# Kernel optimization log

Measured on AMD Instinct MI355X. Metric: run time of the kernel, lower is better.

Reference implementation:

```python
import jax, jax.numpy as jnp
import numpy as np

NUM_EMBEDDINGS = 2048
EMBEDDING_DIM = 64
COMMITMENT_COST = 0.25


def setup_inputs() -> dict:
    key = jax.random.key(0)
    k1, k2 = jax.random.split(key)
    inputs = jax.random.normal(k1, (64, 32, 32, EMBEDDING_DIM), dtype=jnp.float32)
    # lecun_uniform-style scale on fan_in = embedding_dim
    limit = np.sqrt(3.0 / EMBEDDING_DIM).astype(np.float32)
    codebook = jax.random.uniform(k2, (EMBEDDING_DIM, NUM_EMBEDDINGS), dtype=jnp.float32,
                                  minval=-limit, maxval=limit)
    return {"inputs": inputs, "codebook": codebook}


def reference(inputs, codebook):
    lax = jax.lax
    flat = jnp.reshape(inputs, (-1, EMBEDDING_DIM))          # [N, D]
    # squared Euclidean distances to each code: [N, K]
    distances = (jnp.sum(jnp.square(flat), 1, keepdims=True)
                 - 2.0 * jnp.matmul(flat, codebook)
                 + jnp.sum(jnp.square(codebook), 0, keepdims=True))
    encoding_indices = jnp.argmin(distances, 1)              # [N]
    flat_q = jnp.take(codebook, encoding_indices, axis=1).swapaxes(1, 0)  # [N, D]
    quantized = jnp.reshape(flat_q, inputs.shape)

    codebook_loss = jnp.mean(jnp.square(quantized - lax.stop_gradient(inputs)))
    commitment_loss = COMMITMENT_COST * jnp.mean(
        jnp.square(lax.stop_gradient(quantized) - inputs))

    encodings = jax.nn.one_hot(encoding_indices, NUM_EMBEDDINGS, dtype=jnp.float32)
    avg_probs = jnp.mean(encodings, 0)
    perplexity = jnp.exp(-jnp.sum(avg_probs * jnp.log(avg_probs + 1e-10)))

    ste = inputs + lax.stop_gradient(quantized - inputs)
    return (ste, perplexity, codebook_loss, commitment_loss)
```

## Files before the change

### kernel.cpp

```cpp
#include <hip/hip_runtime.h>
#include <math.h>

#define KCODES 2048
#define DIM 64
#define NROWS 65536
#define NELEM (NROWS * DIM)

#define WS_HIST 0
#define WS_C2   8192
#define WS_C2S  16384
#define WS_SSE  24576
#define WS_P    32768

#define EPS_PK 33

typedef float  floatx4 __attribute__((ext_vector_type(4)));
typedef short  short8  __attribute__((ext_vector_type(8)));

__device__ __forceinline__ unsigned short f2bf(float f) {
  union { float f; unsigned u; } a; a.f = f;
  unsigned r = (a.u + 0x7FFFu + ((a.u >> 16) & 1u)) >> 16;
  return (unsigned short)r;
}
__device__ __forceinline__ float bf2f(unsigned short h) {
  union { unsigned u; float f; } a; a.u = ((unsigned)h) << 16;
  return a.f;
}

__global__ void vq_colnorm(const float* __restrict__ cb, float* __restrict__ c2,
                           float* __restrict__ c2s) {
  int k = blockIdx.x * 256 + threadIdx.x;
  float s = 0.f;
#pragma unroll
  for (int d = 0; d < DIM; ++d) {
    float v = cb[d * KCODES + k];
    s = fmaf(v, v, s);
  }
  c2[k] = s;
  c2s[k] = (s + 64.0f) * 16384.0f;
}

__global__ void vq_prep(const float* __restrict__ cb, char* __restrict__ P) {
  int tid = blockIdx.x * 256 + threadIdx.x;
  int code = tid & (KCODES - 1);
  int g = tid >> 11;
  short8 hh, ll;
#pragma unroll
  for (int e = 0; e < 8; ++e) {
    float v = -2.0f * cb[(size_t)(g * 8 + e) * KCODES + code];
    unsigned short hb = f2bf(v);
    float lo = v - bf2f(hb);
    hh[e] = (short)hb;
    ll[e] = (short)f2bf(lo);
  }
  int tile = code >> 5;
  int sn = code & 31;
  int pb = g ^ (sn & 7);
  size_t base = (size_t)tile * 8192 + sn * 128 + pb * 16;
  *(short8*)(P + base) = hh;
  *(short8*)(P + base + 4096) = ll;
}

__device__ __forceinline__ void stage_tile(const char* P, char* lds,
                                           int tile, int w, int lane) {
  const char* gp = P + (size_t)tile * 8192 + w * 1024 + lane * 16;
  char* lp = lds + w * 1024 + lane * 16;
  __builtin_amdgcn_global_load_lds(
      (const __attribute__((address_space(1))) unsigned*)gp,
      (__attribute__((address_space(3))) unsigned*)lp, 16, 0, 0);
  __builtin_amdgcn_global_load_lds(
      (const __attribute__((address_space(1))) unsigned*)(gp + 4096),
      (__attribute__((address_space(3))) unsigned*)(lp + 4096), 16, 0, 0);
}

__global__ __launch_bounds__(256, 2) void vq_main(
    const float* __restrict__ inp, const float* __restrict__ cb,
    const float* __restrict__ c2, const float* __restrict__ c2s,
    const char* __restrict__ P, int* __restrict__ hist,
    float* __restrict__ sse, float* __restrict__ out)
{
  __shared__ __align__(16) char Bstage[2][8192];
  __shared__ float s_c2s[KCODES];
  __shared__ int   s_k[128];
  __shared__ int   s_nflag;
  __shared__ int   s_frows[128];
  __shared__ float s_rd[256];
  __shared__ int   s_rk[256];
  __shared__ float s_red[4];

  const int t    = threadIdx.x;
  const int lane = t & 63;
  const int wave = __builtin_amdgcn_readfirstlane(t >> 6);
  const int c    = lane & 15;
  const int q    = lane >> 4;
  const int c7   = c & 7;
  const int rowbase = blockIdx.x * 128 + wave * 32;

  if (t == 0) s_nflag = 0;

#pragma unroll
  for (int i = 0; i < KCODES / 256; ++i) s_c2s[i * 256 + t] = c2s[i * 256 + t];

  short8 Ah[2][2], Al[2][2];
#pragma unroll
  for (int r = 0; r < 2; ++r) {
#pragma unroll
    for (int s = 0; s < 2; ++s) {
      const float* px = inp + (size_t)(rowbase + r * 16 + c) * 64 + s * 32 + q * 8;
      float4 u0 = *(const float4*)px;
      float4 u1 = *(const float4*)(px + 4);
      float u[8] = {u0.x, u0.y, u0.z, u0.w, u1.x, u1.y, u1.z, u1.w};
      short8 hh, ll;
#pragma unroll
      for (int e = 0; e < 8; ++e) {
        float xs = u[e] * 16384.0f;
        unsigned short hb = f2bf(xs);
        float lo = xs - bf2f(hb);
        hh[e] = (short)hb;
        ll[e] = (short)f2bf(lo);
      }
      Ah[r][s] = hh; Al[r][s] = ll;
    }
  }

  unsigned d1[8], d2[8];
#pragma unroll
  for (int i = 0; i < 8; ++i) { d1[i] = 0xFFFFFFFFu; d2[i] = 0xFFFFFFFFu; }

  stage_tile(P, Bstage[0], 0, wave, lane);
  __syncthreads();

  const floatx4 zero = {0.f, 0.f, 0.f, 0.f};

#pragma unroll 2
  for (int j = 0; j < 64; ++j) {
    const int buf = j & 1;
    if (j + 1 < 64) stage_tile(P, Bstage[1 - buf], j + 1, wave, lane);

    float c2v0 = s_c2s[j * 32 + c];
    float c2v1 = s_c2s[j * 32 + 16 + c];

#pragma unroll
    for (int nt = 0; nt < 2; ++nt) {
      const int rowi = nt * 16 + c;
      const char* bp = &Bstage[buf][rowi * 128];
      short8 bh0 = *(const short8*)(bp + ((0 + q) ^ c7) * 16);
      short8 bh1 = *(const short8*)(bp + ((4 + q) ^ c7) * 16);
      short8 bl0 = *(const short8*)(bp + 4096 + ((0 + q) ^ c7) * 16);
      short8 bl1 = *(const short8*)(bp + 4096 + ((4 + q) ^ c7) * 16);
      const float c2v = nt ? c2v1 : c2v0;
      const unsigned kcn = j * 32 + nt * 16 + c;
#pragma unroll
      for (int r = 0; r < 2; ++r) {
        floatx4 acc = __builtin_amdgcn_mfma_f32_16x16x32_bf16(Al[r][1], bh1, zero, 0, 0, 0);
        acc = __builtin_amdgcn_mfma_f32_16x16x32_bf16(Ah[r][1], bl1, acc, 0, 0, 0);
        acc = __builtin_amdgcn_mfma_f32_16x16x32_bf16(Al[r][0], bh0, acc, 0, 0, 0);
        acc = __builtin_amdgcn_mfma_f32_16x16x32_bf16(Ah[r][0], bl0, acc, 0, 0, 0);
        acc = __builtin_amdgcn_mfma_f32_16x16x32_bf16(Ah[r][1], bh1, acc, 0, 0, 0);
        acc = __builtin_amdgcn_mfma_f32_16x16x32_bf16(Ah[r][0], bh0, acc, 0, 0, 0);
#pragma unroll
        for (int reg = 0; reg < 4; ++reg) {
          float dds = acc[reg] + c2v;
          unsigned u = (((unsigned)dds) << 11) + kcn;
          const int i = r * 4 + reg;
          d2[i] = min(d2[i], max(d1[i], u));
          d1[i] = min(d1[i], u);
        }
      }
    }
    __syncthreads();
  }

#pragma unroll
  for (int i = 0; i < 8; ++i) {
    unsigned D1 = d1[i], D2 = d2[i];
#pragma unroll
    for (int off = 1; off < 16; off <<= 1) {
      unsigned o1 = (unsigned)__shfl_xor((int)D1, off, 64);
      unsigned o2 = (unsigned)__shfl_xor((int)D2, off, 64);
      D2 = min(min(D2, o2), max(D1, o1));
      D1 = min(D1, o1);
    }
    if (c == 0) {
      int lrow = wave * 32 + (i >> 2) * 16 + q * 4 + (i & 3);
      s_k[lrow] = (int)(D1 & 2047u);
      if ((int)((D2 >> 11) - (D1 >> 11)) < EPS_PK) {
        int idx = atomicAdd(&s_nflag, 1);
        s_frows[idx] = lrow;
      }
    }
  }
  __syncthreads();

  const int nf = s_nflag;
  for (int f = 0; f < nf; ++f) {
    const int lrow = s_frows[f];
    const float* xr = inp + (size_t)(blockIdx.x * 128 + lrow) * 64;
    float xs[64];
    float x2 = 0.f;
#pragma unroll
    for (int i = 0; i < 16; ++i) {
      float4 v = *(const float4*)(xr + i * 4);
      xs[4 * i + 0] = v.x; xs[4 * i + 1] = v.y; xs[4 * i + 2] = v.z; xs[4 * i + 3] = v.w;
      x2 = fmaf(v.x, v.x, x2); x2 = fmaf(v.y, v.y, x2);
      x2 = fmaf(v.z, v.z, x2); x2 = fmaf(v.w, v.w, x2);
    }
    float dot[8];
#pragma unroll
    for (int cc = 0; cc < 8; ++cc) dot[cc] = 0.f;
    const float* cp = cb + t * 8;
#pragma unroll 4
    for (int d = 0; d < 64; ++d) {
      float xd = xs[d];
#pragma unroll
      for (int cc = 0; cc < 8; ++cc)
        dot[cc] = fmaf(xd, cp[(size_t)d * KCODES + cc], dot[cc]);
    }
    float bd = INFINITY; int bk = 0;
#pragma unroll
    for (int cc = 0; cc < 8; ++cc) {
      float dd = (x2 - 2.0f * dot[cc]) + c2[t * 8 + cc];
      if (dd < bd) { bd = dd; bk = t * 8 + cc; }
    }
    s_rd[t] = bd; s_rk[t] = bk;
    __syncthreads();
    for (int s = 128; s >= 1; s >>= 1) {
      if (t < s) {
        if (s_rd[t + s] < s_rd[t]) { s_rd[t] = s_rd[t + s]; s_rk[t] = s_rk[t + s]; }
      }
      __syncthreads();
    }
    if (t == 0) s_k[lrow] = s_rk[0];
    __syncthreads();
  }

  if (t < 128) atomicAdd(&hist[s_k[t]], 1);

  const int fr = t >> 1;
  const int fd = (t & 1) * 32;
  const int grow = blockIdx.x * 128 + fr;
  const int myk = s_k[fr];
  const float* xrow = inp + (size_t)grow * 64 + fd;
  float* orow = out + (size_t)grow * 64 + fd;
  float serr = 0.f;
#pragma unroll
  for (int i = 0; i < 32; ++i) {
    float xv = xrow[i];
    float qv = cb[(size_t)(fd + i) * KCODES + myk];
    float dq = qv - xv;
    serr = fmaf(dq, dq, serr);
    orow[i] = xv + dq;
  }
#pragma unroll
  for (int off = 32; off > 0; off >>= 1) serr += __shfl_down(serr, off, 64);
  if (lane == 0) s_red[wave] = serr;
  __syncthreads();
  if (t == 0) atomicAdd(sse, s_red[0] + s_red[1] + s_red[2] + s_red[3]);
}

__global__ void vq_final(const int* __restrict__ hist,
                         const float* __restrict__ sse,
                         float* __restrict__ out) {
  __shared__ float s_red[4];
  const int t = threadIdx.x;
  float s = 0.f;
  for (int k = t; k < KCODES; k += 256) {
    float p = (float)hist[k] * (1.0f / NROWS);
    s += p * logf(p + 1e-10f);
  }
#pragma unroll
  for (int off = 32; off > 0; off >>= 1) s += __shfl_down(s, off, 64);
  if ((t & 63) == 0) s_red[t >> 6] = s;
  __syncthreads();
  if (t == 0) {
    float tot = s_red[0] + s_red[1] + s_red[2] + s_red[3];
    out[NELEM] = expf(-tot);
    float cl = *sse * (1.0f / NELEM);
    out[NELEM + 1] = cl;
    out[NELEM + 2] = 0.25f * cl;
  }
}

extern "C" void kernel_launch(void* const* d_in, const int* in_sizes, int n_in,
                              void* d_out, int out_size, void* d_ws, size_t ws_size,
                              hipStream_t stream) {
  const float* inp = (const float*)d_in[0];
  const float* cb  = (const float*)d_in[1];
  float* out = (float*)d_out;
  char* ws = (char*)d_ws;
  int*   hist = (int*)(ws + WS_HIST);
  float* c2   = (float*)(ws + WS_C2);
  float* c2s  = (float*)(ws + WS_C2S);
  float* sse  = (float*)(ws + WS_SSE);
  char*  P    = ws + WS_P;

  hipMemsetAsync(d_ws, 0, WS_SSE + 16, stream);
  vq_colnorm<<<KCODES / 256, 256, 0, stream>>>(cb, c2, c2s);
  vq_prep<<<KCODES * 8 / 256, 256, 0, stream>>>(cb, P);
  vq_main<<<NROWS / 128, 256, 0, stream>>>(inp, cb, c2, c2s, P, hist, sse, out);
  vq_final<<<1, 256, 0, stream>>>(hist, sse, out);
}
```

Baseline: 188.8 us.

## Load codebook fragments directly into registers and fuse setup, final kernels

Replaces LDS double-buffered staging of the bf16 codebook with a fragment-ordered layout that each lane reads straight from global memory into registers, double-buffered in software, with no per-tile barriers. Folds the column norm into the MFMA accumulator init and merges the two code halves in the top-2 update. Merges colnorm, prep and memset into one setup kernel that also writes a transposed codebook, so the output gather becomes coalesced float4 loads. Drops the final kernel by having the last block, picked with an atomic ticket, compute perplexity and the losses. Register pressure rises and every block rereads the codebook from L2.

```diff
diff --git a/kernel.cpp b/kernel.cpp
--- a/kernel.cpp
+++ b/kernel.cpp
@@ -10,7 +10,9 @@
 #define WS_C2   8192
 #define WS_C2S  16384
 #define WS_SSE  24576
+#define WS_TKT  24580
 #define WS_P    32768
+#define WS_CBT  (32768 + 524288)
 
 #define EPS_PK 33
 
@@ -27,20 +29,10 @@
   return a.f;
 }
 
-__global__ void vq_colnorm(const float* __restrict__ cb, float* __restrict__ c2,
-                           float* __restrict__ c2s) {
-  int k = blockIdx.x * 256 + threadIdx.x;
-  float s = 0.f;
-#pragma unroll
-  for (int d = 0; d < DIM; ++d) {
-    float v = cb[d * KCODES + k];
-    s = fmaf(v, v, s);
-  }
-  c2[k] = s;
-  c2s[k] = (s + 64.0f) * 16384.0f;
-}
-
-__global__ void vq_prep(const float* __restrict__ cb, char* __restrict__ P) {
+__global__ void vq_setup(const float* __restrict__ cb, float* __restrict__ c2,
+                         float* __restrict__ c2s, char* __restrict__ P,
+                         float* __restrict__ cbT, int* __restrict__ hist,
+                         float* __restrict__ sse, int* __restrict__ ticket) {
   int tid = blockIdx.x * 256 + threadIdx.x;
   int code = tid & (KCODES - 1);
   int g = tid >> 11;
@@ -54,32 +46,47 @@
     ll[e] = (short)f2bf(lo);
   }
   int tile = code >> 5;
-  int sn = code & 31;
-  int pb = g ^ (sn & 7);
-  size_t base = (size_t)tile * 8192 + sn * 128 + pb * 16;
-  *(short8*)(P + base) = hh;
-  *(short8*)(P + base + 4096) = ll;
-}
-
-__device__ __forceinline__ void stage_tile(const char* P, char* lds,
-                                           int tile, int w, int lane) {
-  const char* gp = P + (size_t)tile * 8192 + w * 1024 + lane * 16;
-  char* lp = lds + w * 1024 + lane * 16;
-  __builtin_amdgcn_global_load_lds(
-      (const __attribute__((address_space(1))) unsigned*)gp,
-      (__attribute__((address_space(3))) unsigned*)lp, 16, 0, 0);
-  __builtin_amdgcn_global_load_lds(
-      (const __attribute__((address_space(1))) unsigned*)(gp + 4096),
-      (__attribute__((address_space(3))) unsigned*)(lp + 4096), 16, 0, 0);
+  int nt = (code >> 4) & 1;
+  int c = code & 15;
+  int s = g >> 2, q = g & 3;
+  int lane = q * 16 + c;
+  char* base = P + ((size_t)((tile * 2 + nt) * 4 + s)) * 1024 + lane * 16;
+  *(short8*)base = hh;
+  *(short8*)(base + 2048) = ll;
+
+  if (g == 0) {
+    float ssum = 0.f;
+    float* dst = cbT + (size_t)code * 64;
+#pragma unroll
+    for (int d4 = 0; d4 < 16; ++d4) {
+      float4 w;
+      w.x = cb[(size_t)(d4 * 4 + 0) * KCODES + code];
+      w.y = cb[(size_t)(d4 * 4 + 1) * KCODES + code];
+      w.z = cb[(size_t)(d4 * 4 + 2) * KCODES + code];
+      w.w = cb[(size_t)(d4 * 4 + 3) * KCODES + code];
+      ssum = fmaf(w.x, w.x, ssum);
+      ssum = fmaf(w.y, w.y, ssum);
+      ssum = fmaf(w.z, w.z, ssum);
+      ssum = fmaf(w.w, w.w, ssum);
+      *(float4*)(dst + d4 * 4) = w;
+    }
+    c2[code] = ssum;
+    c2s[code] = (ssum + 64.0f) * 16384.0f;
+  } else if (g == 2) {
+    hist[code] = 0;
+  } else if (g == 3 && code == 0) {
+    *sse = 0.f;
+    *ticket = 0;
+  }
 }
 
 __global__ __launch_bounds__(256, 2) void vq_main(
     const float* __restrict__ inp, const float* __restrict__ cb,
     const float* __restrict__ c2, const float* __restrict__ c2s,
-    const char* __restrict__ P, int* __restrict__ hist,
-    float* __restrict__ sse, float* __restrict__ out)
+    const char* __restrict__ P, const float* __restrict__ cbT,
+    int* __restrict__ hist, float* __restrict__ sse,
+    int* __restrict__ ticket, float* __restrict__ out)
 {
-  __shared__ __align__(16) char Bstage[2][8192];
   __shared__ float s_c2s[KCODES];
   __shared__ int   s_k[128];
   __shared__ int   s_nflag;
@@ -87,13 +94,13 @@
   __shared__ float s_rd[256];
   __shared__ int   s_rk[256];
   __shared__ float s_red[4];
+  __shared__ int   s_last;
 
   const int t    = threadIdx.x;
   const int lane = t & 63;
   const int wave = __builtin_amdgcn_readfirstlane(t >> 6);
   const int c    = lane & 15;
   const int q    = lane >> 4;
-  const int c7   = c & 7;
   const int rowbase = blockIdx.x * 128 + wave * 32;
 
   if (t == 0) s_nflag = 0;
@@ -127,49 +134,71 @@
 #pragma unroll
   for (int i = 0; i < 8; ++i) { d1[i] = 0xFFFFFFFFu; d2[i] = 0xFFFFFFFFu; }
 
-  stage_tile(P, Bstage[0], 0, wave, lane);
-  __syncthreads();
-
-  const floatx4 zero = {0.f, 0.f, 0.f, 0.f};
-
-#pragma unroll 2
-  for (int j = 0; j < 64; ++j) {
-    const int buf = j & 1;
-    if (j + 1 < 64) stage_tile(P, Bstage[1 - buf], j + 1, wave, lane);
-
-    float c2v0 = s_c2s[j * 32 + c];
-    float c2v1 = s_c2s[j * 32 + 16 + c];
-
-#pragma unroll
-    for (int nt = 0; nt < 2; ++nt) {
-      const int rowi = nt * 16 + c;
-      const char* bp = &Bstage[buf][rowi * 128];
-      short8 bh0 = *(const short8*)(bp + ((0 + q) ^ c7) * 16);
-      short8 bh1 = *(const short8*)(bp + ((4 + q) ^ c7) * 16);
-      short8 bl0 = *(const short8*)(bp + 4096 + ((0 + q) ^ c7) * 16);
-      short8 bl1 = *(const short8*)(bp + 4096 + ((4 + q) ^ c7) * 16);
-      const float c2v = nt ? c2v1 : c2v0;
-      const unsigned kcn = j * 32 + nt * 16 + c;
-#pragma unroll
-      for (int r = 0; r < 2; ++r) {
-        floatx4 acc = __builtin_amdgcn_mfma_f32_16x16x32_bf16(Al[r][1], bh1, zero, 0, 0, 0);
-        acc = __builtin_amdgcn_mfma_f32_16x16x32_bf16(Ah[r][1], bl1, acc, 0, 0, 0);
-        acc = __builtin_amdgcn_mfma_f32_16x16x32_bf16(Al[r][0], bh0, acc, 0, 0, 0);
-        acc = __builtin_amdgcn_mfma_f32_16x16x32_bf16(Ah[r][0], bl0, acc, 0, 0, 0);
-        acc = __builtin_amdgcn_mfma_f32_16x16x32_bf16(Ah[r][1], bh1, acc, 0, 0, 0);
-        acc = __builtin_amdgcn_mfma_f32_16x16x32_bf16(Ah[r][0], bh0, acc, 0, 0, 0);
-#pragma unroll
-        for (int reg = 0; reg < 4; ++reg) {
-          float dds = acc[reg] + c2v;
-          unsigned u = (((unsigned)dds) << 11) + kcn;
-          const int i = r * 4 + reg;
-          d2[i] = min(d2[i], max(d1[i], u));
-          d1[i] = min(d1[i], u);
-        }
-      }
-    }
-    __syncthreads();
-  }
+  const char* Pl = P + lane * 16;
+
+#define LOADJ(DST, jj) do {                                         \
+    const char* p0_ = Pl + (size_t)(jj) * 8192;                     \
+    const char* p1_ = p0_ + 4096;                                   \
+    DST[0] = *(const short8*)(p0_);                                 \
+    DST[1] = *(const short8*)(p0_ + 1024);                          \
+    DST[2] = *(const short8*)(p0_ + 2048);                          \
+    DST[3] = *(const short8*)(p0_ + 3072);                          \
+    DST[4] = *(const short8*)(p1_);                                 \
+    DST[5] = *(const short8*)(p1_ + 1024);                          \
+    DST[6] = *(const short8*)(p1_ + 2048);                          \
+    DST[7] = *(const short8*)(p1_ + 3072);                          \
+  } while (0)
+
+#define COMPUTE(BB, j) do {                                                              \
+    const float c2v0 = s_c2s[(j) * 32 + c];                                              \
+    const float c2v1 = s_c2s[(j) * 32 + 16 + c];                                         \
+    const floatx4 ca0 = {c2v0, c2v0, c2v0, c2v0};                                        \
+    const floatx4 ca1 = {c2v1, c2v1, c2v1, c2v1};                                        \
+    const unsigned kc0 = (unsigned)((j) * 32 + c);                                       \
+    _Pragma("unroll")                                                                    \
+    for (int r = 0; r < 2; ++r) {                                                        \
+      floatx4 a0 = __builtin_amdgcn_mfma_f32_16x16x32_bf16(Al[r][1], BB[1], ca0, 0,0,0); \
+      a0 = __builtin_amdgcn_mfma_f32_16x16x32_bf16(Ah[r][1], BB[3], a0, 0,0,0);          \
+      a0 = __builtin_amdgcn_mfma_f32_16x16x32_bf16(Al[r][0], BB[0], a0, 0,0,0);          \
+      a0 = __builtin_amdgcn_mfma_f32_16x16x32_bf16(Ah[r][0], BB[2], a0, 0,0,0);          \
+      a0 = __builtin_amdgcn_mfma_f32_16x16x32_bf16(Ah[r][1], BB[1], a0, 0,0,0);          \
+      a0 = __builtin_amdgcn_mfma_f32_16x16x32_bf16(Ah[r][0], BB[0], a0, 0,0,0);          \
+      floatx4 a1 = __builtin_amdgcn_mfma_f32_16x16x32_bf16(Al[r][1], BB[5], ca1, 0,0,0); \
+      a1 = __builtin_amdgcn_mfma_f32_16x16x32_bf16(Ah[r][1], BB[7], a1, 0,0,0);          \
+      a1 = __builtin_amdgcn_mfma_f32_16x16x32_bf16(Al[r][0], BB[4], a1, 0,0,0);          \
+      a1 = __builtin_amdgcn_mfma_f32_16x16x32_bf16(Ah[r][0], BB[6], a1, 0,0,0);          \
+      a1 = __builtin_amdgcn_mfma_f32_16x16x32_bf16(Ah[r][1], BB[5], a1, 0,0,0);          \
+      a1 = __builtin_amdgcn_mfma_f32_16x16x32_bf16(Ah[r][0], BB[4], a1, 0,0,0);          \
+      _Pragma("unroll")                                                                  \
+      for (int reg = 0; reg < 4; ++reg) {                                                \
+        unsigned u0 = (((unsigned)a0[reg]) << 11) + kc0;                                 \
+        unsigned u1 = (((unsigned)a1[reg]) << 11) + kc0 + 16u;                           \
+        unsigned mn = min(u0, u1), mx = max(u0, u1);                                     \
+        const int i = r * 4 + reg;                                                       \
+        d2[i] = min(min(max(d1[i], mn), mx), d2[i]);                                     \
+        d1[i] = min(d1[i], mn);                                                          \
+      }                                                                                  \
+    }                                                                                    \
+  } while (0)
+
+  short8 B0[8], B1[8];
+  LOADJ(B0, 0);
+  __syncthreads();
+
+#pragma unroll 1
+  for (int jj = 0; jj < 31; ++jj) {
+    const int j0 = 2 * jj;
+    LOADJ(B1, j0 + 1);
+    COMPUTE(B0, j0);
+    LOADJ(B0, j0 + 2);
+    COMPUTE(B1, j0 + 1);
+  }
+  LOADJ(B1, 63);
+  COMPUTE(B0, 62);
+  COMPUTE(B1, 63);
+
+#undef COMPUTE
+#undef LOADJ
 
 #pragma unroll
   for (int i = 0; i < 8; ++i) {
@@ -236,48 +265,51 @@
 
   if (t < 128) atomicAdd(&hist[s_k[t]], 1);
 
-  const int fr = t >> 1;
-  const int fd = (t & 1) * 32;
-  const int grow = blockIdx.x * 128 + fr;
-  const int myk = s_k[fr];
-  const float* xrow = inp + (size_t)grow * 64 + fd;
-  float* orow = out + (size_t)grow * 64 + fd;
+  const float* xb = inp + (size_t)blockIdx.x * (128 * 64);
+  float* ob = out + (size_t)blockIdx.x * (128 * 64);
   float serr = 0.f;
 #pragma unroll
-  for (int i = 0; i < 32; ++i) {
-    float xv = xrow[i];
-    float qv = cb[(size_t)(fd + i) * KCODES + myk];
-    float dq = qv - xv;
-    serr = fmaf(dq, dq, serr);
-    orow[i] = xv + dq;
+  for (int i = 0; i < 8; ++i) {
+    const int idx = i * 1024 + t * 4;
+    const int myk = s_k[idx >> 6];
+    const float4 xv = *(const float4*)(xb + idx);
+    const float4 qv = *(const float4*)(cbT + (size_t)myk * 64 + (idx & 63));
+    float4 ov;
+    float e0 = qv.x - xv.x; serr = fmaf(e0, e0, serr); ov.x = xv.x + e0;
+    float e1 = qv.y - xv.y; serr = fmaf(e1, e1, serr); ov.y = xv.y + e1;
+    float e2 = qv.z - xv.z; serr = fmaf(e2, e2, serr); ov.z = xv.z + e2;
+    float e3 = qv.w - xv.w; serr = fmaf(e3, e3, serr); ov.w = xv.w + e3;
+    *(float4*)(ob + idx) = ov;
   }
 #pragma unroll
   for (int off = 32; off > 0; off >>= 1) serr += __shfl_down(serr, off, 64);
   if (lane == 0) s_red[wave] = serr;
   __syncthreads();
   if (t == 0) atomicAdd(sse, s_red[0] + s_red[1] + s_red[2] + s_red[3]);
-}
-
-__global__ void vq_final(const int* __restrict__ hist,
-                         const float* __restrict__ sse,
-                         float* __restrict__ out) {
-  __shared__ float s_red[4];
-  const int t = threadIdx.x;
-  float s = 0.f;
-  for (int k = t; k < KCODES; k += 256) {
-    float p = (float)hist[k] * (1.0f / NROWS);
-    s += p * logf(p + 1e-10f);
-  }
-#pragma unroll
-  for (int off = 32; off > 0; off >>= 1) s += __shfl_down(s, off, 64);
-  if ((t & 63) == 0) s_red[t >> 6] = s;
-  __syncthreads();
-  if (t == 0) {
-    float tot = s_red[0] + s_red[1] + s_red[2] + s_red[3];
-    out[NELEM] = expf(-tot);
-    float cl = *sse * (1.0f / NELEM);
-    out[NELEM + 1] = cl;
-    out[NELEM + 2] = 0.25f * cl;
+
+  __threadfence();
+  __syncthreads();
+  if (t == 0) s_last = (atomicAdd(ticket, 1) == (int)gridDim.x - 1) ? 1 : 0;
+  __syncthreads();
+  if (s_last) {
+    float s = 0.f;
+    for (int k = t; k < KCODES; k += 256) {
+      int h = atomicAdd(&hist[k], 0);
+      float p = (float)h * (1.0f / NROWS);
+      s += p * logf(p + 1e-10f);
+    }
+#pragma unroll
+    for (int off = 32; off > 0; off >>= 1) s += __shfl_down(s, off, 64);
+    if (lane == 0) s_red[wave] = s;
+    __syncthreads();
+    if (t == 0) {
+      float tot = s_red[0] + s_red[1] + s_red[2] + s_red[3];
+      float sv = atomicAdd(sse, 0.0f);
+      out[NELEM] = expf(-tot);
+      float cl = sv * (1.0f / NELEM);
+      out[NELEM + 1] = cl;
+      out[NELEM + 2] = 0.25f * cl;
+    }
   }
 }
 
@@ -292,11 +324,10 @@
   float* c2   = (float*)(ws + WS_C2);
   float* c2s  = (float*)(ws + WS_C2S);
   float* sse  = (float*)(ws + WS_SSE);
+  int*   tkt  = (int*)(ws + WS_TKT);
   char*  P    = ws + WS_P;
-
-  hipMemsetAsync(d_ws, 0, WS_SSE + 16, stream);
-  vq_colnorm<<<KCODES / 256, 256, 0, stream>>>(cb, c2, c2s);
-  vq_prep<<<KCODES * 8 / 256, 256, 0, stream>>>(cb, P);
-  vq_main<<<NROWS / 128, 256, 0, stream>>>(inp, cb, c2, c2s, P, hist, sse, out);
-  vq_final<<<1, 256, 0, stream>>>(hist, sse, out);
-}
+  float* cbT  = (float*)(ws + WS_CBT);
+
+  vq_setup<<<KCODES * 8 / 256, 256, 0, stream>>>(cb, c2, c2s, P, cbT, hist, sse, tkt);
+  vq_main<<<NROWS / 128, 256, 0, stream>>>(inp, cb, c2, c2s, P, cbT, hist, sse, tkt, out);
+}
```

Result: slower. 209.7 us (+11.1%).
